# Optimization experiments

Measured on AMD Instinct MI355X. Metric: run time of the kernel, lower is better.

The kernel has to match this reference:

```python
import jax, jax.numpy as jnp
import numpy as np
from jax import lax

NUM_HEADS = 8


def setup_inputs() -> dict:
    key = jax.random.key(0)
    ks = jax.random.split(key, 6)
    B, L, Hd = 4, 4096, 512
    S = 45  # factor * ceil(ln(L)) = 5 * 9
    x = jax.random.normal(ks[0], (B, L, Hd), dtype=jnp.float32)
    scale = 1.0 / np.sqrt(Hd)
    Wq = jax.random.normal(ks[1], (Hd, Hd), dtype=jnp.float32) * scale
    Wk = jax.random.normal(ks[2], (Hd, Hd), dtype=jnp.float32) * scale
    Wv = jax.random.normal(ks[3], (Hd, Hd), dtype=jnp.float32) * scale
    Wo = jax.random.normal(ks[4], (Hd, Hd), dtype=jnp.float32) * scale
    index_sample = jax.random.randint(ks[5], (L, S), 0, L, dtype=jnp.int32)
    return {"x": x, "Wq": Wq, "Wk": Wk, "Wv": Wv, "Wo": Wo,
            "index_sample": index_sample}


def reference(x, Wq, Wk, Wv, Wo, index_sample):
    B, L, Hd = x.shape
    H = NUM_HEADS
    D = Hd // H
    S = index_sample.shape[1]
    u = S  # n_top active queries = factor*ceil(ln(L))

    def split_heads(t):  # [B,L,Hd] -> [B,H,L,D]
        return t.reshape(B, L, H, D).transpose(0, 2, 1, 3)

    q = split_heads(x @ Wq)
    k = split_heads(x @ Wk)
    v = split_heads(x @ Wv)

    scale = 1.0 / jnp.sqrt(jnp.asarray(D, dtype=x.dtype))

    # sampled key gather: [B,H,L,S,D]
    K_samp = k[:, :, index_sample, :]
    # sampled scores per query: [B,H,L,S]
    QK_samp = jnp.einsum('bhld,bhlsd->bhls', q, K_samp)
    # sparsity measurement: max - mean over sampled keys
    M = QK_samp.max(axis=-1) - QK_samp.mean(axis=-1)  # [B,H,L]
    _, top_idx = lax.top_k(M, u)                      # [B,H,u]

    # full attention only for active queries
    Qr = jnp.take_along_axis(q, top_idx[..., None], axis=2)   # [B,H,u,D]
    scores = jnp.einsum('bhud,bhld->bhul', Qr, k) * scale     # [B,H,u,L]
    attn = jax.nn.softmax(scores, axis=-1)
    ctx_sel = jnp.einsum('bhul,bhld->bhud', attn, v)          # [B,H,u,D]

    # inactive queries get mean(V); scatter active results in
    context = jnp.broadcast_to(v.mean(axis=2, keepdims=True), (B, H, L, D))
    b_idx = jnp.arange(B)[:, None, None]
    h_idx = jnp.arange(H)[None, :, None]
    context = context.at[b_idx, h_idx, top_idx].set(ctx_sel)

    out = context.transpose(0, 2, 1, 3).reshape(B, L, Hd) @ Wo
    return out
```

## Files before the change

### kernel.cpp

```cpp
#include <hip/hip_runtime.h>
#include <cmath>

#define SS 45
#define FSPLIT 16

typedef __attribute__((ext_vector_type(8))) _Float16 half8;
typedef __attribute__((ext_vector_type(4))) float float4v;
typedef __attribute__((ext_vector_type(8))) unsigned short ushort8v;

__device__ inline unsigned short f16b(float f) {
    union { _Float16 h; unsigned short u; } c;
    c.h = (_Float16)f;
    return c.u;
}
__device__ inline float f16back(unsigned short u) {
    union { _Float16 h; unsigned short u; } c;
    c.u = u;
    return (float)c.h;
}

__device__ __forceinline__ void async16(const void* g, void* l) {
    __builtin_amdgcn_global_load_lds(
        (const __attribute__((address_space(1))) void*)g,
        (__attribute__((address_space(3))) void*)l, 16, 0, 0);
}

template <int CTRL>
__device__ __forceinline__ float dppadd(float v) {
    int x = __builtin_amdgcn_mov_dpp(__float_as_int(v), CTRL, 0xF, 0xF, true);
    return v + __int_as_float(x);
}
template <int CTRL>
__device__ __forceinline__ float dppmax(float v) {
    int x = __builtin_amdgcn_mov_dpp(__float_as_int(v), CTRL, 0xF, 0xF, true);
    return fmaxf(v, __int_as_float(x));
}

__device__ __forceinline__ unsigned int fmono(float f) {
    unsigned int u = __float_as_uint(f);
    return (u & 0x80000000u) ? ~u : (u | 0x80000000u);
}

__global__ __launch_bounds__(256) void convW_kernel(
    const float* __restrict__ Wq, const float* __restrict__ Wk, const float* __restrict__ Wv,
    unsigned short* __restrict__ WTh, unsigned short* __restrict__ WTl,
    float* __restrict__ vmp)
{
    int bid = blockIdx.x;
    if (bid < 768) {
        int zy = bid >> 8;
        int bxy = bid & 255;
        const float* W = (zy == 0) ? Wq : (zy == 1) ? Wk : Wv;
        unsigned short* th = WTh + (size_t)zy * 262144;
        unsigned short* tl = WTl + (size_t)zy * 262144;
        __shared__ float t[32][33];
        int bx = bxy & 15, by = bxy >> 4;
        int tx = threadIdx.x & 31, ty = threadIdx.x >> 5;
        for (int i = ty; i < 32; i += 8) t[i][tx] = W[(size_t)(by * 32 + i) * 512 + bx * 32 + tx];
        __syncthreads();
        for (int i = ty; i < 32; i += 8) {
            float f = t[tx][i];
            unsigned short h = f16b(f);
            unsigned short lo = f16b(f - f16back(h));
            th[(size_t)(bx * 32 + i) * 512 + by * 32 + tx] = h;
            tl[(size_t)(bx * 32 + i) * 512 + by * 32 + tx] = lo;
        }
    } else {
        for (int i = threadIdx.x; i < 2048; i += 256) vmp[i] = 0.f;
    }
}

__global__ __launch_bounds__(512, 2) void qkv8_kernel(
    const float* __restrict__ X,
    const unsigned short* __restrict__ WTh, const unsigned short* __restrict__ WTl,
    float* __restrict__ Q, float* __restrict__ K, float* __restrict__ V,
    float* __restrict__ vmp)
{
    __shared__ unsigned short lds[73728];

    int wave = threadIdx.x >> 6;
    int lane = threadIdx.x & 63;
    int m0blk = blockIdx.x * 256;
    int n0blk = blockIdx.y * 128;
    int fr = lane & 15;
    int C = lane >> 4;
    int srow = lane >> 2;
    int sslot = lane & 3;
    int mrb = (wave >> 1) * 64;
    int nrb = (wave & 1) * 64;

    const unsigned short* gbB[5];
    gbB[0] = WTh;
    gbB[1] = WTl;
    gbB[2] = WTh + 262144;
    gbB[3] = WTl + 262144;
    gbB[4] = WTh + 524288;

    int rloc0 = wave * 32 + srow;
    int rloc1 = wave * 32 + 16 + srow;
    int Cp0 = sslot ^ ((rloc0 >> 1) & 3);
    int Cp1 = sslot ^ ((rloc1 >> 1) & 3);
    const float* xr0 = X + (size_t)(m0blk + rloc0) * 512 + Cp0 * 8;
    const float* xr1 = X + (size_t)(m0blk + rloc1) * 512 + Cp1 * 8;

    float4v accq[4][4], acck[4][4], accv[4][4];
    #pragma unroll
    for (int i = 0; i < 4; i++)
        #pragma unroll
        for (int j = 0; j < 4; j++) {
            accq[i][j] = (float4v){0.f, 0.f, 0.f, 0.f};
            acck[i][j] = (float4v){0.f, 0.f, 0.f, 0.f};
            accv[i][j] = (float4v){0.f, 0.f, 0.f, 0.f};
        }

    auto stageB = [&](int buf, int k0) {
        int rloc = wave * 16 + srow;
        int Cp = sslot ^ ((rloc >> 1) & 3);
        #pragma unroll
        for (int t = 0; t < 5; t++) {
            const unsigned short* g = gbB[t] + (size_t)(n0blk + rloc) * 512 + k0 + Cp * 8;
            async16(g, lds + buf * 36864 + 16384 + t * 4096 + wave * 512);
        }
    };

    float4 xv[2][2];
    auto loadX = [&](int k0) {
        xv[0][0] = *(const float4*)(xr0 + k0);
        xv[0][1] = *(const float4*)(xr0 + k0 + 4);
        xv[1][0] = *(const float4*)(xr1 + k0);
        xv[1][1] = *(const float4*)(xr1 + k0 + 4);
    };
    auto writeA = [&](int buf) {
        #pragma unroll
        for (int inst = 0; inst < 2; inst++) {
            const float* f = (const float*)&xv[inst][0];
            ushort8v hv, lv;
            #pragma unroll
            for (int e = 0; e < 8; e++) {
                unsigned short h = f16b(f[e]);
                hv[e] = h;
                lv[e] = f16b(f[e] - f16back(h));
            }
            unsigned short* dsth = lds + buf * 36864 + (wave * 32 + inst * 16) * 32 + lane * 8;
            *(ushort8v*)dsth = hv;
            *(ushort8v*)(dsth + 8192) = lv;
        }
    };

    loadX(0);
    stageB(0, 0);
    writeA(0);
    asm volatile("s_waitcnt vmcnt(0)" ::: "memory");
    asm volatile("s_waitcnt lgkmcnt(0)" ::: "memory");
    __builtin_amdgcn_s_barrier();

    for (int kk = 0; kk < 16; kk++) {
        const unsigned short* Lb = lds + (kk & 1) * 36864;
        int nbuf = (kk + 1) & 1;
        int nk0 = (kk + 1) * 32;

        if (kk < 15) {
            loadX(nk0);
            stageB(nbuf, nk0);
        }

        half8 A_h[4], A_l[4];
        #pragma unroll
        for (int i = 0; i < 4; i++) {
            int R = mrb + i * 16 + fr;
            int sl = C ^ ((R >> 1) & 3);
            A_h[i] = *(const half8*)(Lb + R * 32 + sl * 8);
            A_l[i] = *(const half8*)(Lb + 8192 + R * 32 + sl * 8);
        }
        #pragma unroll
        for (int j = 0; j < 4; j++) {
            int R = nrb + j * 16 + fr;
            int sl = C ^ ((R >> 1) & 3);
            int off = R * 32 + sl * 8;
            half8 Bqh = *(const half8*)(Lb + 16384 + off);
            half8 Bql = *(const half8*)(Lb + 20480 + off);
            half8 Bkh = *(const half8*)(Lb + 24576 + off);
            half8 Bkl = *(const half8*)(Lb + 28672 + off);
            half8 Bvh = *(const half8*)(Lb + 32768 + off);
            #pragma unroll
            for (int i = 0; i < 4; i++) {
                accq[i][j] = __builtin_amdgcn_mfma_f32_16x16x32_f16(A_h[i], Bqh, accq[i][j], 0, 0, 0);
                accq[i][j] = __builtin_amdgcn_mfma_f32_16x16x32_f16(A_h[i], Bql, accq[i][j], 0, 0, 0);
                accq[i][j] = __builtin_amdgcn_mfma_f32_16x16x32_f16(A_l[i], Bqh, accq[i][j], 0, 0, 0);
                acck[i][j] = __builtin_amdgcn_mfma_f32_16x16x32_f16(A_h[i], Bkh, acck[i][j], 0, 0, 0);
                acck[i][j] = __builtin_amdgcn_mfma_f32_16x16x32_f16(A_h[i], Bkl, acck[i][j], 0, 0, 0);
                acck[i][j] = __builtin_amdgcn_mfma_f32_16x16x32_f16(A_l[i], Bkh, acck[i][j], 0, 0, 0);
                accv[i][j] = __builtin_amdgcn_mfma_f32_16x16x32_f16(A_h[i], Bvh, accv[i][j], 0, 0, 0);
            }
        }

        if (kk < 15) {
            writeA(nbuf);
            asm volatile("s_waitcnt vmcnt(0)" ::: "memory");
            asm volatile("s_waitcnt lgkmcnt(0)" ::: "memory");
            __builtin_amdgcn_s_barrier();
        }
    }

    int hh = n0blk + nrb;
    int hd = hh >> 6;
    int bb0 = (m0blk + mrb) >> 12;
    {
        float cs[4];
        #pragma unroll
        for (int j = 0; j < 4; j++) {
            float s = 0.f;
            #pragma unroll
            for (int i = 0; i < 4; i++)
                #pragma unroll
                for (int r = 0; r < 4; r++) s += accv[i][j][r];
            s += __shfl_xor(s, 16, 64);
            s += __shfl_xor(s, 32, 64);
            cs[j] = s;
        }
        if (C == 0) {
            #pragma unroll
            for (int j = 0; j < 4; j++)
                atomicAdd(vmp + ((size_t)(bb0 * 8 + hd) * 64) + j * 16 + fr, cs[j]);
        }
    }

    int rbase = C * 4;
    int m0 = m0blk + mrb;
    #pragma unroll
    for (int i = 0; i < 4; i++)
        #pragma unroll
        for (int r = 0; r < 4; r++) {
            int rg = m0 + i * 16 + rbase + r;
            int bb = rg >> 12, l = rg & 4095;
            size_t rowoff = ((size_t)(bb * 8 + hd) * 4096 + l) * 64;
            #pragma unroll
            for (int j = 0; j < 4; j++) Q[rowoff + j * 16 + fr] = accq[i][j][r];
            #pragma unroll
            for (int j = 0; j < 4; j++) K[rowoff + j * 16 + fr] = acck[i][j][r];
            #pragma unroll
            for (int j = 0; j < 4; j++) V[rowoff + j * 16 + fr] = accv[i][j][r];
        }
}

__global__ __launch_bounds__(256) void m_kernel(
    const float* __restrict__ Q, const float* __restrict__ K,
    const int* __restrict__ idx, float* __restrict__ M)
{
    int wave = threadIdx.x >> 6;
    int lane = threadIdx.x & 63;
    int g = lane >> 3;
    int t = lane & 7;
    int inst0 = blockIdx.x * 16 + wave * 4;
    for (int ii = 0; ii < 4; ii++) {
        int inst = inst0 + ii;
        int bh = inst >> 12;
        int l = inst & 4095;
        float4 qa = *(const float4*)(Q + (size_t)inst * 64 + t * 4);
        float4 qb = *(const float4*)(Q + (size_t)inst * 64 + 32 + t * 4);
        const float* kb = K + (size_t)bh * 4096 * 64;
        const int* irow = idx + (size_t)l * SS;
        int jv[6];
        #pragma unroll
        for (int it = 0; it < 6; it++) {
            int s = it * 8 + g;
            jv[it] = irow[(it == 5 && g >= 5) ? 0 : s];
        }
        float4 kva[6], kvb[6];
        #pragma unroll
        for (int it = 0; it < 6; it++) {
            kva[it] = *(const float4*)(kb + (size_t)jv[it] * 64 + t * 4);
            kvb[it] = *(const float4*)(kb + (size_t)jv[it] * 64 + 32 + t * 4);
        }
        float maxv = -1e30f, sum = 0.f, p0 = 0.f;
        #pragma unroll
        for (int it = 0; it < 6; it++) {
            float p = qa.x * kva[it].x;
            p = fmaf(qa.y, kva[it].y, p);
            p = fmaf(qa.z, kva[it].z, p);
            p = fmaf(qa.w, kva[it].w, p);
            p = fmaf(qb.x, kvb[it].x, p);
            p = fmaf(qb.y, kvb[it].y, p);
            p = fmaf(qb.z, kvb[it].z, p);
            p = fmaf(qb.w, kvb[it].w, p);
            p = dppadd<0xB1>(p);
            p = dppadd<0x4E>(p);
            p = dppadd<0x141>(p);
            if (it == 0) p0 = p;
            maxv = fmaxf(maxv, p);
            sum += p;
        }
        maxv = dppmax<0x128>(maxv);
        maxv = fmaxf(maxv, __shfl_xor(maxv, 16, 64));
        maxv = fmaxf(maxv, __shfl_xor(maxv, 32, 64));
        sum = dppadd<0x128>(sum);
        sum += __shfl_xor(sum, 16, 64);
        sum += __shfl_xor(sum, 32, 64);
        float p0b = __shfl(p0, 0, 64);
        if (lane == 0) M[inst] = maxv - (sum - 3.f * p0b) * (1.f / 45.f);
    }
}

__global__ __launch_bounds__(256) void topk_local_kernel(
    const float* __restrict__ M, unsigned long long* __restrict__ cand)
{
    int chunk = blockIdx.x;
    int bh = chunk >> 3, c = chunk & 7;
    __shared__ unsigned long long keys[512];
    int tid = threadIdx.x;
    for (int i = tid; i < 512; i += 256) {
        int l = c * 512 + i;
        unsigned int u = fmono(M[(size_t)bh * 4096 + l]);
        keys[i] = ((unsigned long long)u << 32) | (unsigned int)(4095 - l);
    }
    __syncthreads();
    for (int k = 2; k <= 512; k <<= 1)
        for (int j = k >> 1; j > 0; j >>= 1) {
            for (int i0 = tid; i0 < 512; i0 += 256) {
                int ixj = i0 ^ j;
                if (ixj > i0) {
                    unsigned long long a = keys[i0], b = keys[ixj];
                    bool asc = (i0 & k) != 0;
                    if (asc ? (a > b) : (a < b)) { keys[i0] = b; keys[ixj] = a; }
                }
            }
            __syncthreads();
        }
    if (tid < SS) cand[(size_t)chunk * SS + tid] = keys[tid];
}

__global__ __launch_bounds__(256) void topk_merge_base_kernel(
    const unsigned long long* __restrict__ cand, int* __restrict__ tidx,
    const float* __restrict__ vmp, const float* __restrict__ Wo,
    float* __restrict__ vmean, float* __restrict__ base)
{
    int bid = blockIdx.x;
    int tid = threadIdx.x;
    if (bid < 32) {
        __shared__ unsigned long long keys[512];
        for (int i = tid; i < 512; i += 256) {
            unsigned long long v = 0ull;
            if (i < 8 * SS) {
                int cc = i / SS, r = i - cc * SS;
                v = cand[((size_t)bid * 8 + cc) * SS + r];
            }
            keys[i] = v;
        }
        __syncthreads();
        for (int k = 2; k <= 512; k <<= 1)
            for (int j = k >> 1; j > 0; j >>= 1) {
                for (int i0 = tid; i0 < 512; i0 += 256) {
                    int ixj = i0 ^ j;
                    if (ixj > i0) {
                        unsigned long long a = keys[i0], b = keys[ixj];
                        bool asc = (i0 & k) != 0;
                        if (asc ? (a > b) : (a < b)) { keys[i0] = b; keys[ixj] = a; }
                    }
                }
                __syncthreads();
            }
        if (tid < SS) tidx[bid * SS + tid] = 4095 - (int)(keys[tid] & 0xFFFFFFFFu);
    } else {
        int b = bid - 32;
        __shared__ float vmS[512];
        for (int i = tid; i < 512; i += 256) {
            float s = vmp[(size_t)b * 512 + i] * (1.f / 4096.f);
            vmS[i] = s;
            vmean[(size_t)b * 512 + i] = s;
        }
        __syncthreads();
        for (int jj = tid; jj < 512; jj += 256) {
            float s = 0.f;
            for (int i = 0; i < 512; i++) s += vmS[i] * Wo[(size_t)i * 512 + jj];
            base[(size_t)b * 512 + jj] = s;
        }
    }
}

__global__ __launch_bounds__(256) void attn_fill_kernel(
    const float* __restrict__ Q, const float* __restrict__ K, const float* __restrict__ V,
    const int* __restrict__ tidx,
    float* __restrict__ Opart, float* __restrict__ mpart, float* __restrict__ lpart,
    const float4* __restrict__ base4, float4* __restrict__ out4)
{
    int bid = blockIdx.x;
    if (bid >= 512) {
        int i0 = (bid - 512) * 1024 + threadIdx.x;
        #pragma unroll
        for (int k = 0; k < 4; k++) {
            int i = i0 + k * 256;
            int b = i >> 19;
            int j4 = i & 127;
            out4[i] = base4[b * 128 + j4];
        }
        return;
    }
    int split = bid & 15;
    int bh = bid >> 4;
    int L0 = split * (4096 / FSPLIT);

    __shared__ float Qs[48][68];
    __shared__ float Ks[64][68];
    __shared__ float Vs[64][68];
    __shared__ float Ps[48][68];
    __shared__ int tS[48];

    int tid = threadIdx.x;
    int lane = tid & 63, w = tid >> 6;
    if (tid < 48) tS[tid] = (tid < SS) ? tidx[bh * SS + tid] : 0;
    __syncthreads();
    for (int u = w; u < 48; u += 4)
        Qs[u][lane] = Q[((size_t)bh * 4096 + tS[u]) * 64 + lane];

    int ug = tid >> 4, lg = tid & 15;
    float mrun[3], lrun[3], O[3][4];
    #pragma unroll
    for (int i = 0; i < 3; i++) {
        mrun[i] = -1e30f; lrun[i] = 0.f;
        #pragma unroll
        for (int j = 0; j < 4; j++) O[i][j] = 0.f;
    }

    for (int tt = 0; tt < 4096 / FSPLIT / 64; tt++) {
        int lbase = L0 + tt * 64;
        if (tt > 0) __syncthreads();
        for (int r = w; r < 64; r += 4) {
            Ks[r][lane] = K[((size_t)bh * 4096 + lbase + r) * 64 + lane];
            Vs[r][lane] = V[((size_t)bh * 4096 + lbase + r) * 64 + lane];
        }
        __syncthreads();

        {
            float acc[3][4];
            #pragma unroll
            for (int i = 0; i < 3; i++)
                #pragma unroll
                for (int j = 0; j < 4; j++) acc[i][j] = 0.f;
            for (int d0 = 0; d0 < 64; d0 += 4) {
                float4 a[3], b[4];
                #pragma unroll
                for (int i = 0; i < 3; i++) a[i] = *(float4*)&Qs[ug * 3 + i][d0];
                #pragma unroll
                for (int j = 0; j < 4; j++) b[j] = *(float4*)&Ks[lg * 4 + j][d0];
                #pragma unroll
                for (int i = 0; i < 3; i++)
                    #pragma unroll
                    for (int j = 0; j < 4; j++)
                        acc[i][j] += a[i].x * b[j].x + a[i].y * b[j].y + a[i].z * b[j].z + a[i].w * b[j].w;
            }
            #pragma unroll
            for (int i = 0; i < 3; i++) {
                #pragma unroll
                for (int j = 0; j < 4; j++) acc[i][j] *= 0.125f;
                float tm = fmaxf(fmaxf(acc[i][0], acc[i][1]), fmaxf(acc[i][2], acc[i][3]));
                tm = fmaxf(tm, __shfl_xor(tm, 1, 64));
                tm = fmaxf(tm, __shfl_xor(tm, 2, 64));
                tm = fmaxf(tm, __shfl_xor(tm, 4, 64));
                tm = fmaxf(tm, __shfl_xor(tm, 8, 64));
                float nm = fmaxf(mrun[i], tm);
                float corr = __expf(mrun[i] - nm);
                float rs = 0.f;
                #pragma unroll
                for (int j = 0; j < 4; j++) {
                    float p = __expf(acc[i][j] - nm);
                    Ps[ug * 3 + i][lg * 4 + j] = p;
                    rs += p;
                }
                rs += __shfl_xor(rs, 1, 64);
                rs += __shfl_xor(rs, 2, 64);
                rs += __shfl_xor(rs, 4, 64);
                rs += __shfl_xor(rs, 8, 64);
                lrun[i] = lrun[i] * corr + rs;
                mrun[i] = nm;
                #pragma unroll
                for (int j = 0; j < 4; j++) O[i][j] *= corr;
            }
        }
        __syncthreads();

        {
            for (int l0 = 0; l0 < 64; l0 += 4) {
                float4 vr[4];
                #pragma unroll
                for (int r = 0; r < 4; r++) vr[r] = *(float4*)&Vs[l0 + r][lg * 4];
                #pragma unroll
                for (int i = 0; i < 3; i++) {
                    float4 pv = *(float4*)&Ps[ug * 3 + i][l0];
                    #pragma unroll
                    for (int j = 0; j < 4; j++) {
                        float vj0 = (&vr[0].x)[j], vj1 = (&vr[1].x)[j];
                        float vj2 = (&vr[2].x)[j], vj3 = (&vr[3].x)[j];
                        O[i][j] = fmaf(pv.x, vj0, fmaf(pv.y, vj1, fmaf(pv.z, vj2, fmaf(pv.w, vj3, O[i][j]))));
                    }
                }
            }
        }
    }

    {
        #pragma unroll
        for (int i = 0; i < 3; i++) {
            int u = ug * 3 + i;
            if (u < SS) {
                size_t pbase = ((size_t)(bh * FSPLIT + split) * SS + u);
                if (lg == 0) { mpart[pbase] = mrun[i]; lpart[pbase] = lrun[i]; }
                #pragma unroll
                for (int j = 0; j < 4; j++)
                    Opart[pbase * 64 + lg * 4 + j] = O[i][j];
            }
        }
    }
}

__global__ __launch_bounds__(256) void combine_kernel(
    const float* __restrict__ Opart, const float* __restrict__ mpart, const float* __restrict__ lpart,
    const float* __restrict__ vmean, const float* __restrict__ Wo,
    const int* __restrict__ tidx, float* __restrict__ out)
{
    int rr = blockIdx.x;
    int bh = rr / SS, u = rr % SS;
    int h = bh & 7, b = bh >> 3;
    __shared__ float dS[64];
    int tid = threadIdx.x;
    if (tid < 64) {
        float m = -1e30f;
        #pragma unroll
        for (int s = 0; s < FSPLIT; s++)
            m = fmaxf(m, mpart[(size_t)(bh * FSPLIT + s) * SS + u]);
        float den = 0.f, num = 0.f;
        #pragma unroll
        for (int s = 0; s < FSPLIT; s++) {
            size_t pbase = (size_t)(bh * FSPLIT + s) * SS + u;
            float wgt = __expf(mpart[pbase] - m);
            den += wgt * lpart[pbase];
            num += wgt * Opart[pbase * 64 + tid];
        }
        dS[tid] = num / den - vmean[(size_t)bh * 64 + tid];
    }
    __syncthreads();
    int l = tidx[rr];
    float* orow = out + ((size_t)b * 4096 + l) * 512;
    for (int j = tid; j < 512; j += 256) {
        float s = 0.f;
        #pragma unroll
        for (int dd = 0; dd < 64; dd++) s += dS[dd] * Wo[(size_t)(h * 64 + dd) * 512 + j];
        atomicAdd(orow + j, s);
    }
}

extern "C" void kernel_launch(void* const* d_in, const int* in_sizes, int n_in,
                              void* d_out, int out_size, void* d_ws, size_t ws_size,
                              hipStream_t stream)
{
    const float* x  = (const float*)d_in[0];
    const float* Wq = (const float*)d_in[1];
    const float* Wk = (const float*)d_in[2];
    const float* Wv = (const float*)d_in[3];
    const float* Wo = (const float*)d_in[4];
    const int*  idx = (const int*)d_in[5];
    float* out = (float*)d_out;

    float* W = (float*)d_ws;
    float* Q = W;
    float* K = W + 8388608;
    float* V = W + 16777216;
    unsigned short* WTh = (unsigned short*)(W + 33554432);
    unsigned short* WTl = (unsigned short*)(W + 33947648);
    float* vmp = W + 34340864;

    float* Mv    = W + 25165824;
    float* Opart = W + 25296896;
    float* mpart = W + 26771456;
    float* lpart = W + 26794496;
    float* vmean = W + 33439744;
    float* base  = W + 33441792;
    int*   tidx  = (int*)(W + 33443840);
    unsigned long long* cand = (unsigned long long*)(W + 33445280);

    convW_kernel<<<769, 256, 0, stream>>>(Wq, Wk, Wv, WTh, WTl, vmp);
    qkv8_kernel<<<dim3(64, 4), 512, 0, stream>>>(x, WTh, WTl, Q, K, V, vmp);
    m_kernel<<<8192, 256, 0, stream>>>(Q, K, idx, Mv);
    topk_local_kernel<<<256, 256, 0, stream>>>(Mv, cand);
    topk_merge_base_kernel<<<36, 256, 0, stream>>>(cand, tidx, vmp, Wo, vmean, base);
    attn_fill_kernel<<<512 + 2048, 256, 0, stream>>>(Q, K, V, tidx, Opart, mpart, lpart,
                                                     (const float4*)base, (float4*)out);
    combine_kernel<<<1440, 256, 0, stream>>>(Opart, mpart, lpart, vmean, Wo, tidx, out);
}
```

Before: 405.0 us.

## Fuse sparsity-measure computation with local top-k sort into one kernel

```diff
diff --git a/kernel.cpp b/kernel.cpp
--- a/kernel.cpp
+++ b/kernel.cpp
@@ -243,22 +243,25 @@
         }
 }
 
-__global__ __launch_bounds__(256) void m_kernel(
+__global__ __launch_bounds__(1024) void m_topk_kernel(
     const float* __restrict__ Q, const float* __restrict__ K,
-    const int* __restrict__ idx, float* __restrict__ M)
-{
+    const int* __restrict__ idx, unsigned long long* __restrict__ cand)
+{
+    __shared__ unsigned long long keys[512];
+
+    int bh = blockIdx.x & 31;
+    int c = blockIdx.x >> 5;
     int wave = threadIdx.x >> 6;
     int lane = threadIdx.x & 63;
     int g = lane >> 3;
     int t = lane & 7;
-    int inst0 = blockIdx.x * 16 + wave * 4;
-    for (int ii = 0; ii < 4; ii++) {
-        int inst = inst0 + ii;
-        int bh = inst >> 12;
-        int l = inst & 4095;
+    const float* kb = K + (size_t)bh * 4096 * 64;
+
+    for (int ii = 0; ii < 32; ii++) {
+        int l = c * 512 + wave * 32 + ii;
+        int inst = bh * 4096 + l;
         float4 qa = *(const float4*)(Q + (size_t)inst * 64 + t * 4);
         float4 qb = *(const float4*)(Q + (size_t)inst * 64 + 32 + t * 4);
-        const float* kb = K + (size_t)bh * 4096 * 64;
         const int* irow = idx + (size_t)l * SS;
         int jv[6];
         #pragma unroll
@@ -297,26 +300,19 @@
         sum += __shfl_xor(sum, 16, 64);
         sum += __shfl_xor(sum, 32, 64);
         float p0b = __shfl(p0, 0, 64);
-        if (lane == 0) M[inst] = maxv - (sum - 3.f * p0b) * (1.f / 45.f);
-    }
-}
-
-__global__ __launch_bounds__(256) void topk_local_kernel(
-    const float* __restrict__ M, unsigned long long* __restrict__ cand)
-{
-    int chunk = blockIdx.x;
-    int bh = chunk >> 3, c = chunk & 7;
-    __shared__ unsigned long long keys[512];
+        if (lane == 0) {
+            float Mval = maxv - (sum - 3.f * p0b) * (1.f / 45.f);
+            keys[wave * 32 + ii] =
+                ((unsigned long long)fmono(Mval) << 32) | (unsigned int)(4095 - l);
+        }
+    }
+    __syncthreads();
+
     int tid = threadIdx.x;
-    for (int i = tid; i < 512; i += 256) {
-        int l = c * 512 + i;
-        unsigned int u = fmono(M[(size_t)bh * 4096 + l]);
-        keys[i] = ((unsigned long long)u << 32) | (unsigned int)(4095 - l);
-    }
-    __syncthreads();
     for (int k = 2; k <= 512; k <<= 1)
         for (int j = k >> 1; j > 0; j >>= 1) {
-            for (int i0 = tid; i0 < 512; i0 += 256) {
+            if (tid < 512) {
+                int i0 = tid;
                 int ixj = i0 ^ j;
                 if (ixj > i0) {
                     unsigned long long a = keys[i0], b = keys[ixj];
@@ -326,7 +322,7 @@
             }
             __syncthreads();
         }
-    if (tid < SS) cand[(size_t)chunk * SS + tid] = keys[tid];
+    if (tid < SS) cand[((size_t)bh * 8 + c) * SS + tid] = keys[tid];
 }
 
 __global__ __launch_bounds__(256) void topk_merge_base_kernel(
@@ -568,7 +564,6 @@
     unsigned short* WTl = (unsigned short*)(W + 33947648);
     float* vmp = W + 34340864;
 
-    float* Mv    = W + 25165824;
     float* Opart = W + 25296896;
     float* mpart = W + 26771456;
     float* lpart = W + 26794496;
@@ -579,8 +574,7 @@
 
     convW_kernel<<<769, 256, 0, stream>>>(Wq, Wk, Wv, WTh, WTl, vmp);
     qkv8_kernel<<<dim3(64, 4), 512, 0, stream>>>(x, WTh, WTl, Q, K, V, vmp);
-    m_kernel<<<8192, 256, 0, stream>>>(Q, K, idx, Mv);
-    topk_local_kernel<<<256, 256, 0, stream>>>(Mv, cand);
+    m_topk_kernel<<<256, 1024, 0, stream>>>(Q, K, idx, cand);
     topk_merge_base_kernel<<<36, 256, 0, stream>>>(cand, tidx, vmp, Wo, vmean, base);
     attn_fill_kernel<<<512 + 2048, 256, 0, stream>>>(Q, K, V, tidx, Opart, mpart, lpart,
                                                      (const float4*)base, (float4*)out);
```

Measured after the change: 386.1 us. 4.7% less time.
